# Kernel tuning notes

Measured on AMD Instinct MI355X. Metric: run time of the kernel, lower is better.

Reference implementation:

```python
import jax, jax.numpy as jnp
import numpy as np

DIM = 64
NUM_NODES = 64
SEQ_LEN = 256
BATCH = 64


def setup_inputs() -> dict:
    key = jax.random.key(0)
    ks = jax.random.split(key, 8)
    D = DIM
    x = jax.random.normal(ks[0], (SEQ_LEN, BATCH, NUM_NODES, D), dtype=jnp.float32)
    mask = jnp.ones((SEQ_LEN,), dtype=jnp.int32)
    # msg MLP: Linear(3D -> D) + GELU
    lim_msg = 1.0 / np.sqrt(3 * D)
    msg_W = jax.random.uniform(ks[1], (D, 3 * D), minval=-lim_msg, maxval=lim_msg, dtype=jnp.float32)
    msg_b = jax.random.uniform(ks[2], (D,), minval=-lim_msg, maxval=lim_msg, dtype=jnp.float32)
    # GRUCell(input=D, hidden=D); torch init U(-1/sqrt(hidden), 1/sqrt(hidden))
    lim_g = 1.0 / np.sqrt(D)
    W_ih = jax.random.uniform(ks[3], (3 * D, D), minval=-lim_g, maxval=lim_g, dtype=jnp.float32)
    W_hh = jax.random.uniform(ks[4], (3 * D, D), minval=-lim_g, maxval=lim_g, dtype=jnp.float32)
    b_ih = jax.random.uniform(ks[5], (3 * D,), minval=-lim_g, maxval=lim_g, dtype=jnp.float32)
    b_hh = jax.random.uniform(ks[6], (3 * D,), minval=-lim_g, maxval=lim_g, dtype=jnp.float32)
    # TimeEncode params
    basis_freq = jnp.asarray(1.0 / 10.0 ** np.linspace(0, 9, D), dtype=jnp.float32)
    phase = jnp.zeros((D,), dtype=jnp.float32)
    return {"x": x, "mask": mask, "msg_W": msg_W, "msg_b": msg_b,
            "W_ih": W_ih, "W_hh": W_hh, "b_ih": b_ih, "b_hh": b_hh,
            "basis_freq": basis_freq, "phase": phase}


def _forward(x, mask, msg_W, msg_b, W_ih, W_hh, b_ih, b_hh, basis_freq, phase):
    T, B, C, D = x.shape
    # TimeEncode: cos(t * freq + phase) -> [T, D]
    ts = jnp.arange(T, dtype=jnp.float32)[:, None]
    t_enc = jnp.cos(ts * basis_freq[None, :] + phase[None, :])
    # init_func == 'mean': mean over time -> [B, C, D] -> [B*C, D]
    s0 = jnp.mean(x, axis=0).reshape(B * C, D)
    # time_range = arange(T) * mask (gather indices)
    tr = jnp.arange(T) * mask.astype(jnp.int32)
    x_seq = x[tr].reshape(T, B * C, D)      # gathered timesteps
    te_seq = t_enc[tr]                       # [T, D]

    def step(s, inp):
        xt, tt = inp                        # xt: [B*C, D], tt: [D]
        tt_b = jnp.broadcast_to(tt[None, :], xt.shape)
        cat = jnp.concatenate([xt, s, tt_b], axis=-1)  # [B*C, 3D]
        msg = jax.nn.gelu(cat @ msg_W.T + msg_b, approximate=False)
        # GRUCell (torch gate order: r, z, n)
        gi = msg @ W_ih.T + b_ih
        gh = s @ W_hh.T + b_hh
        i_r, i_z, i_n = jnp.split(gi, 3, axis=-1)
        h_r, h_z, h_n = jnp.split(gh, 3, axis=-1)
        r = jax.nn.sigmoid(i_r + h_r)
        z = jax.nn.sigmoid(i_z + h_z)
        n = jnp.tanh(i_n + r * h_n)
        s_new = (1.0 - z) * n + z * s
        return s_new, s_new

    _, states = jax.lax.scan(step, s0, (x_seq, te_seq))
    return states.reshape(T, B, C, D)


def reference(x, mask, msg_W, msg_b, W_ih, W_hh, b_ih, b_hh, basis_freq, phase):
    return _forward(x, mask, msg_W, msg_b, W_ih, W_hh, b_ih, b_hh, basis_freq, phase)
```

## Files before the change

kernel.cpp:

```cpp
#include <hip/hip_runtime.h>
#include <math.h>

#define DD    64
#define TT    256
#define NROW  4096
#define BLK   512
#define GRID  256

typedef __attribute__((ext_vector_type(8))) short  short8;
typedef __attribute__((ext_vector_type(4))) float  f32x4;

#define BARRIER() do {                                        \
    asm volatile("s_waitcnt lgkmcnt(0)" ::: "memory");        \
    __builtin_amdgcn_sched_barrier(0);                        \
    __builtin_amdgcn_s_barrier();                             \
    __builtin_amdgcn_sched_barrier(0);                        \
  } while (0)

__device__ __forceinline__ unsigned short f2bf(float f) {
  unsigned u = __builtin_bit_cast(unsigned, f);
  u += 0x7fffu + ((u >> 16) & 1u);
  return (unsigned short)(u >> 16);
}

__device__ __forceinline__ unsigned long long pack4(float4 v) {
  return (unsigned long long)f2bf(v.x)
       | ((unsigned long long)f2bf(v.y) << 16)
       | ((unsigned long long)f2bf(v.z) << 32)
       | ((unsigned long long)f2bf(v.w) << 48);
}

__device__ __forceinline__ short8 load_wfrag(const float* p) {
  float4 a = *(const float4*)p;
  float4 b = *(const float4*)(p + 4);
  short8 r;
  r[0] = (short)f2bf(a.x); r[1] = (short)f2bf(a.y);
  r[2] = (short)f2bf(a.z); r[3] = (short)f2bf(a.w);
  r[4] = (short)f2bf(b.x); r[5] = (short)f2bf(b.y);
  r[6] = (short)f2bf(b.z); r[7] = (short)f2bf(b.w);
  return r;
}

__device__ __forceinline__ float fsigmoid(float x) {
  return __builtin_amdgcn_rcpf(1.0f + __expf(-x));
}
__device__ __forceinline__ float ftanh(float x) {
  return 1.0f - 2.0f * __builtin_amdgcn_rcpf(1.0f + __expf(2.0f * x));
}
__device__ __forceinline__ float ferf(float x) {
  float ax = fabsf(x);
  float t  = __builtin_amdgcn_rcpf(fmaf(0.3275911f, ax, 1.0f));
  float p  = fmaf(1.061405429f, t, -1.453152027f);
  p = fmaf(p, t, 1.421413741f);
  p = fmaf(p, t, -0.284496736f);
  p = fmaf(p, t, 0.254829592f);
  p = p * t;
  float y = 1.0f - p * __expf(-ax * ax);
  return copysignf(y, x);
}

__global__ void bias_kernel(const float* __restrict__ msg_W,
                            const float* __restrict__ msg_b,
                            const float* __restrict__ freq,
                            const float* __restrict__ phase,
                            float* __restrict__ bias_t) {
  __shared__ float teL[DD];
  const int t = blockIdx.x;
  const int j = threadIdx.x;
  teL[j] = cosf(fmaf((float)t, freq[j], phase[j]));
  __syncthreads();
  float acc = msg_b[j];
  const float* wrow = msg_W + j * 192 + 128;
  #pragma unroll 8
  for (int k = 0; k < DD; ++k) acc = fmaf(teL[k], wrow[k], acc);
  bias_t[t * DD + j] = acc;
}

__launch_bounds__(BLK, 1)
__global__ void scan5(const float* __restrict__ x,
                      const int*   __restrict__ mask,
                      const float* __restrict__ msg_W,
                      const float* __restrict__ W_ih,
                      const float* __restrict__ W_hh,
                      const float* __restrict__ b_ih,
                      const float* __restrict__ b_hh,
                      const float* __restrict__ bias_t,
                      float* __restrict__ out) {
  __shared__ alignas(16) unsigned short xs[2][16 * 72];
  __shared__ alignas(16) unsigned short ss[16 * 72];
  __shared__ alignas(16) unsigned short ms[16 * 72];
  __shared__ alignas(16) float s0a[16 * 68];
  __shared__ alignas(16) float ghl[16 * 260];
  __shared__ int tr_lds[TT + 2];

  const int tid  = threadIdx.x;
  const int lane = tid & 63;
  const int wv   = tid >> 6;
  const int grp  = wv >> 2;
  const int w4   = wv & 3;
  const int col  = lane & 15;
  const int kh   = lane >> 4;
  const int n    = w4 * 16 + col;
  const int row0 = blockIdx.x * 16;

  if (tid < TT) tr_lds[tid] = tid * mask[tid];
  else if (tid < TT + 2) tr_lds[tid] = 0;

  short8 wm[4], wi[3][2], wh[3][2];
  float bsum01[2] = {0.f, 0.f}, bih2 = 0.f, bhh2 = 0.f;
  if (grp == 0) {
    const float* mrow = msg_W + (size_t)n * 192;
    #pragma unroll
    for (int kf = 0; kf < 4; ++kf) wm[kf] = load_wfrag(mrow + kf * 32 + kh * 8);
    #pragma unroll
    for (int p = 0; p < 3; ++p) {
      const float* irow = W_ih + (size_t)(p * 64 + n) * 64;
      #pragma unroll
      for (int kf = 0; kf < 2; ++kf) wi[p][kf] = load_wfrag(irow + kf * 32 + kh * 8);
    }
    bsum01[0] = b_ih[n]      + b_hh[n];
    bsum01[1] = b_ih[64 + n] + b_hh[64 + n];
    bih2 = b_ih[128 + n];
    bhh2 = b_hh[128 + n];
  } else {
    #pragma unroll
    for (int p = 0; p < 3; ++p) {
      const float* hrow = W_hh + (size_t)(p * 64 + n) * 64;
      #pragma unroll
      for (int kf = 0; kf < 2; ++kf) wh[p][kf] = load_wfrag(hrow + kf * 32 + kh * 8);
    }
  }

  {
    const int half = tid >> 8, rem = tid & 255;
    const int fr = rem >> 4, fd = (rem & 15) * 4;
    const float* px = x + ((size_t)half * 128) * (NROW * DD)
                        + (size_t)(row0 + fr) * DD + fd;
    float4 acc = {0.f, 0.f, 0.f, 0.f};
    #pragma unroll 4
    for (int tl = 0; tl < 128; ++tl) {
      float4 v = *(const float4*)(px + (size_t)tl * (NROW * DD));
      acc.x += v.x; acc.y += v.y; acc.z += v.z; acc.w += v.w;
    }
    float* dst = (half == 0) ? &s0a[fr * 68 + fd] : &ghl[fr * 68 + fd];
    *(float4*)dst = acc;
  }
  __syncthreads();
  if (tid < 256) {
    const int fr = tid >> 4, fd = (tid & 15) * 4;
    float4 a = *(const float4*)&s0a[fr * 68 + fd];
    float4 b = *(const float4*)&ghl[fr * 68 + fd];
    const float inv = 1.0f / 256.0f;
    float4 m = { (a.x + b.x) * inv, (a.y + b.y) * inv,
                 (a.z + b.z) * inv, (a.w + b.w) * inv };
    *(float4*)&s0a[fr * 68 + fd] = m;
    *(unsigned long long*)&ss[fr * 72 + fd] = pack4(m);
    float4 xv0 = *(const float4*)(x + (size_t)(row0 + fr) * DD + fd);
    *(unsigned long long*)&xs[0][fr * 72 + fd] = pack4(xv0);
  }
  __syncthreads();

  float s_reg[4] = {0.f, 0.f, 0.f, 0.f};
  float btc = 0.f;
  if (grp == 0) {
    #pragma unroll
    for (int i = 0; i < 4; ++i) s_reg[i] = s0a[(kh * 4 + i) * 68 + n];
    btc = bias_t[n];
    __builtin_amdgcn_s_setprio(1);
  }

  const int t1  = tid & 255;
  const int fr1 = t1 >> 4;
  const int fd1 = (t1 & 15) * 4;
  float4 xv = {0.f, 0.f, 0.f, 0.f};
  if (grp == 1)
    xv = *(const float4*)(x + ((size_t)tr_lds[1] * NROW + row0 + fr1) * DD + fd1);

  for (int t = 0; t < TT; ++t) {
    if (grp == 0) {
      const unsigned short* ax = &xs[t & 1][(lane & 15) * 72];
      const unsigned short* as = &ss[(lane & 15) * 72];
      short8 xa0 = *(const short8*)(ax + kh * 8);
      short8 xa1 = *(const short8*)(ax + 32 + kh * 8);
      short8 sa0 = *(const short8*)(as + kh * 8);
      short8 sa1 = *(const short8*)(as + 32 + kh * 8);
      float btn = 0.f;
      if (t + 1 < TT) btn = bias_t[tr_lds[t + 1] * DD + n];
      f32x4 amx = {0.f, 0.f, 0.f, 0.f};
      amx = __builtin_amdgcn_mfma_f32_16x16x32_bf16(xa0, wm[0], amx, 0, 0, 0);
      amx = __builtin_amdgcn_mfma_f32_16x16x32_bf16(xa1, wm[1], amx, 0, 0, 0);
      f32x4 ams = {0.f, 0.f, 0.f, 0.f};
      ams = __builtin_amdgcn_mfma_f32_16x16x32_bf16(sa0, wm[2], ams, 0, 0, 0);
      ams = __builtin_amdgcn_mfma_f32_16x16x32_bf16(sa1, wm[3], ams, 0, 0, 0);
      #pragma unroll
      for (int i = 0; i < 4; ++i) {
        float a = amx[i] + ams[i] + btc;
        float g = 0.5f * a * (1.0f + ferf(a * 0.70710678118654752f));
        ms[(kh * 4 + i) * 72 + n] = f2bf(g);
      }
      btc = btn;
    } else {
      if (t + 1 < TT)
        *(unsigned long long*)&xs[(t + 1) & 1][fr1 * 72 + fd1] = pack4(xv);
      if (t + 2 < TT)
        xv = *(const float4*)(x + ((size_t)tr_lds[t + 2] * NROW + row0 + fr1) * DD + fd1);
      const unsigned short* as = &ss[(lane & 15) * 72];
      short8 sa0 = *(const short8*)(as + kh * 8);
      short8 sa1 = *(const short8*)(as + 32 + kh * 8);
      f32x4 agh[3];
      #pragma unroll
      for (int p = 0; p < 3; ++p) {
        f32x4 c = {0.f, 0.f, 0.f, 0.f};
        c = __builtin_amdgcn_mfma_f32_16x16x32_bf16(sa0, wh[p][0], c, 0, 0, 0);
        c = __builtin_amdgcn_mfma_f32_16x16x32_bf16(sa1, wh[p][1], c, 0, 0, 0);
        agh[p] = c;
      }
      #pragma unroll
      for (int i = 0; i < 4; ++i) {
        float4 gv = { agh[0][i], agh[1][i], agh[2][i], 0.f };
        *(float4*)&ghl[(kh * 4 + i) * 260 + n * 4] = gv;
      }
    }
    BARRIER();

    if (grp == 0) {
      const unsigned short* am = &ms[(lane & 15) * 72];
      short8 ma0 = *(const short8*)(am + kh * 8);
      short8 ma1 = *(const short8*)(am + 32 + kh * 8);
      f32x4 agi[3];
      #pragma unroll
      for (int p = 0; p < 3; ++p) {
        f32x4 c = {0.f, 0.f, 0.f, 0.f};
        c = __builtin_amdgcn_mfma_f32_16x16x32_bf16(ma0, wi[p][0], c, 0, 0, 0);
        c = __builtin_amdgcn_mfma_f32_16x16x32_bf16(ma1, wi[p][1], c, 0, 0, 0);
        agi[p] = c;
      }
      #pragma unroll
      for (int i = 0; i < 4; ++i) {
        const int rr = kh * 4 + i;
        float4 gh4 = *(const float4*)&ghl[rr * 260 + n * 4];
        float gr  = agi[0][i] + gh4.x + bsum01[0];
        float gz  = agi[1][i] + gh4.y + bsum01[1];
        float gni = agi[2][i] + bih2;
        float gnh = gh4.z + bhh2;
        float rg = fsigmoid(gr);
        float zg = fsigmoid(gz);
        float ng = ftanh(fmaf(rg, gnh, gni));
        float sn = fmaf(zg, s_reg[i] - ng, ng);
        s_reg[i] = sn;
        ss[rr * 72 + n] = f2bf(sn);
        out[((size_t)t * NROW + row0 + rr) * DD + n] = sn;
      }
    }
    BARRIER();
  }
}

extern "C" void kernel_launch(void* const* d_in, const int* in_sizes, int n_in,
                              void* d_out, int out_size, void* d_ws, size_t ws_size,
                              hipStream_t stream) {
  const float* x      = (const float*)d_in[0];
  const int*   mask   = (const int*)  d_in[1];
  const float* msg_W  = (const float*)d_in[2];
  const float* msg_b  = (const float*)d_in[3];
  const float* W_ih   = (const float*)d_in[4];
  const float* W_hh   = (const float*)d_in[5];
  const float* b_ih   = (const float*)d_in[6];
  const float* b_hh   = (const float*)d_in[7];
  const float* freq   = (const float*)d_in[8];
  const float* phase  = (const float*)d_in[9];
  float* out    = (float*)d_out;
  float* bias_t = (float*)d_ws;

  (void)in_sizes; (void)n_in; (void)out_size; (void)ws_size;

  bias_kernel<<<TT, DD, 0, stream>>>(msg_W, msg_b, freq, phase, bias_t);
  scan5<<<GRID, BLK, 0, stream>>>(x, mask, msg_W, W_ih, W_hh,
                                  b_ih, b_hh, bias_t, out);
}
```

Measured before the change: 345.7 us.

## Halve rows per block to double grid, stage outputs through LDS for coalesced stores

Each block now handles 8 rows instead of 16, doubling the grid to 512 blocks so more CUs get work. MFMA tiles stay 16 rows wide, with the upper 8 rows zero-padded. Output stores move from scattered per-element writes in the GRU wave group to coalesced float4 writes by the second wave group, one step later, read from an fp32 LDS copy of the state. The x prefetch moves after the first barrier and drops double buffering. Half of the MFMA work is wasted on padding, and occupancy now depends on register and LDS limits under launch_bounds(512,4).

```diff
diff --git a/kernel.cpp b/kernel.cpp
--- a/kernel.cpp
+++ b/kernel.cpp
@@ -4,8 +4,9 @@
 #define DD    64
 #define TT    256
 #define NROW  4096
+#define RV    8
 #define BLK   512
-#define GRID  256
+#define GRID  (NROW / RV)
 
 typedef __attribute__((ext_vector_type(8))) short  short8;
 typedef __attribute__((ext_vector_type(4))) float  f32x4;
@@ -76,8 +77,8 @@
   bias_t[t * DD + j] = acc;
 }
 
-__launch_bounds__(BLK, 1)
-__global__ void scan5(const float* __restrict__ x,
+__launch_bounds__(BLK, 4)
+__global__ void scan6(const float* __restrict__ x,
                       const int*   __restrict__ mask,
                       const float* __restrict__ msg_W,
                       const float* __restrict__ W_ih,
@@ -86,7 +87,7 @@
                       const float* __restrict__ b_hh,
                       const float* __restrict__ bias_t,
                       float* __restrict__ out) {
-  __shared__ alignas(16) unsigned short xs[2][16 * 72];
+  __shared__ alignas(16) unsigned short xs[16 * 72];
   __shared__ alignas(16) unsigned short ss[16 * 72];
   __shared__ alignas(16) unsigned short ms[16 * 72];
   __shared__ alignas(16) float s0a[16 * 68];
@@ -101,7 +102,7 @@
   const int col  = lane & 15;
   const int kh   = lane >> 4;
   const int n    = w4 * 16 + col;
-  const int row0 = blockIdx.x * 16;
+  const int row0 = blockIdx.x * RV;
 
   if (tid < TT) tr_lds[tid] = tid * mask[tid];
   else if (tid < TT + 2) tr_lds[tid] = 0;
@@ -132,31 +133,39 @@
   }
 
   {
-    const int half = tid >> 8, rem = tid & 255;
-    const int fr = rem >> 4, fd = (rem & 15) * 4;
-    const float* px = x + ((size_t)half * 128) * (NROW * DD)
+    const int q = tid >> 7, u = tid & 127;
+    const int fr = u >> 4, fd = (u & 15) * 4;
+    const float* px = x + ((size_t)(q * 64)) * (NROW * DD)
                         + (size_t)(row0 + fr) * DD + fd;
     float4 acc = {0.f, 0.f, 0.f, 0.f};
     #pragma unroll 4
-    for (int tl = 0; tl < 128; ++tl) {
+    for (int tl = 0; tl < 64; ++tl) {
       float4 v = *(const float4*)(px + (size_t)tl * (NROW * DD));
       acc.x += v.x; acc.y += v.y; acc.z += v.z; acc.w += v.w;
     }
-    float* dst = (half == 0) ? &s0a[fr * 68 + fd] : &ghl[fr * 68 + fd];
-    *(float4*)dst = acc;
+    *(float4*)&ghl[(q * 128 + u) * 4] = acc;
   }
   __syncthreads();
-  if (tid < 256) {
+  if (tid < 128) {
     const int fr = tid >> 4, fd = (tid & 15) * 4;
-    float4 a = *(const float4*)&s0a[fr * 68 + fd];
-    float4 b = *(const float4*)&ghl[fr * 68 + fd];
+    float4 a = *(const float4*)&ghl[tid * 4];
+    float4 b = *(const float4*)&ghl[(128 + tid) * 4];
+    float4 c = *(const float4*)&ghl[(256 + tid) * 4];
+    float4 d = *(const float4*)&ghl[(384 + tid) * 4];
     const float inv = 1.0f / 256.0f;
-    float4 m = { (a.x + b.x) * inv, (a.y + b.y) * inv,
-                 (a.z + b.z) * inv, (a.w + b.w) * inv };
+    float4 m = { (a.x + b.x + c.x + d.x) * inv, (a.y + b.y + c.y + d.y) * inv,
+                 (a.z + b.z + c.z + d.z) * inv, (a.w + b.w + c.w + d.w) * inv };
     *(float4*)&s0a[fr * 68 + fd] = m;
     *(unsigned long long*)&ss[fr * 72 + fd] = pack4(m);
     float4 xv0 = *(const float4*)(x + (size_t)(row0 + fr) * DD + fd);
-    *(unsigned long long*)&xs[0][fr * 72 + fd] = pack4(xv0);
+    *(unsigned long long*)&xs[fr * 72 + fd] = pack4(xv0);
+  } else if (tid < 256) {
+    const int u2 = tid - 128;
+    const int fr = 8 + (u2 >> 4), fd = (u2 & 15) * 4;
+    float4 z = {0.f, 0.f, 0.f, 0.f};
+    *(float4*)&s0a[fr * 68 + fd] = z;
+    *(unsigned long long*)&ss[fr * 72 + fd] = 0ull;
+    *(unsigned long long*)&xs[fr * 72 + fd] = 0ull;
   }
   __syncthreads();
 
@@ -173,12 +182,12 @@
   const int fr1 = t1 >> 4;
   const int fd1 = (t1 & 15) * 4;
   float4 xv = {0.f, 0.f, 0.f, 0.f};
-  if (grp == 1)
+  if (grp == 1 && t1 < 128)
     xv = *(const float4*)(x + ((size_t)tr_lds[1] * NROW + row0 + fr1) * DD + fd1);
 
   for (int t = 0; t < TT; ++t) {
     if (grp == 0) {
-      const unsigned short* ax = &xs[t & 1][(lane & 15) * 72];
+      const unsigned short* ax = &xs[(lane & 15) * 72];
       const unsigned short* as = &ss[(lane & 15) * 72];
       short8 xa0 = *(const short8*)(ax + kh * 8);
       short8 xa1 = *(const short8*)(ax + 32 + kh * 8);
@@ -200,10 +209,6 @@
       }
       btc = btn;
     } else {
-      if (t + 1 < TT)
-        *(unsigned long long*)&xs[(t + 1) & 1][fr1 * 72 + fd1] = pack4(xv);
-      if (t + 2 < TT)
-        xv = *(const float4*)(x + ((size_t)tr_lds[t + 2] * NROW + row0 + fr1) * DD + fd1);
       const unsigned short* as = &ss[(lane & 15) * 72];
       short8 sa0 = *(const short8*)(as + kh * 8);
       short8 sa1 = *(const short8*)(as + 32 + kh * 8);
@@ -219,6 +224,10 @@
       for (int i = 0; i < 4; ++i) {
         float4 gv = { agh[0][i], agh[1][i], agh[2][i], 0.f };
         *(float4*)&ghl[(kh * 4 + i) * 260 + n * 4] = gv;
+      }
+      if (t > 0 && t1 < 128) {
+        float4 ov = *(const float4*)&s0a[fr1 * 68 + fd1];
+        *(float4*)(out + ((size_t)(t - 1) * NROW + row0 + fr1) * DD + fd1) = ov;
       }
     }
     BARRIER();
@@ -248,11 +257,23 @@
         float ng = ftanh(fmaf(rg, gnh, gni));
         float sn = fmaf(zg, s_reg[i] - ng, ng);
         s_reg[i] = sn;
-        ss[rr * 72 + n] = f2bf(sn);
-        out[((size_t)t * NROW + row0 + rr) * DD + n] = sn;
+        ss[rr * 72 + n]  = f2bf(sn);
+        s0a[rr * 68 + n] = sn;
+      }
+    } else {
+      if (t1 < 128) {
+        if (t + 1 < TT)
+          *(unsigned long long*)&xs[fr1 * 72 + fd1] = pack4(xv);
+        if (t + 2 < TT)
+          xv = *(const float4*)(x + ((size_t)tr_lds[t + 2] * NROW + row0 + fr1) * DD + fd1);
       }
     }
     BARRIER();
+  }
+
+  if (grp == 1 && t1 < 128) {
+    float4 ov = *(const float4*)&s0a[fr1 * 68 + fd1];
+    *(float4*)(out + ((size_t)(TT - 1) * NROW + row0 + fr1) * DD + fd1) = ov;
   }
 }
 
@@ -275,6 +296,6 @@
   (void)in_sizes; (void)n_in; (void)out_size; (void)ws_size;
 
   bias_kernel<<<TT, DD, 0, stream>>>(msg_W, msg_b, freq, phase, bias_t);
-  scan5<<<GRID, BLK, 0, stream>>>(x, mask, msg_W, W_ih, W_hh,
+  scan6<<<GRID, BLK, 0, stream>>>(x, mask, msg_W, W_ih, W_hh,
                                   b_ih, b_hh, bias_t, out);
 }
```

After: 377.6 us. +9.2%, slower.

## Move x-projection MFMA and output stores to the second wave group, off the critical path

Applied to the files above, without the earlier changes.

The input projection x_t·W_x plus time bias is now computed by the W_hh wave group one step ahead, during the second phase, and handed over through shared memory. The message phase then only runs the state-dependent MFMAs. Output stores move from scattered per-element writes in the critical group to coalesced float4 writes by the other group, delayed by one step via an fp32 state copy in shared memory. This shortens the serial dependency chain in each recurrent step, at the cost of extra shared-memory traffic.

```diff
diff --git a/kernel.cpp b/kernel.cpp
--- a/kernel.cpp
+++ b/kernel.cpp
@@ -23,22 +23,26 @@
   return (unsigned short)(u >> 16);
 }
 
-__device__ __forceinline__ unsigned long long pack4(float4 v) {
-  return (unsigned long long)f2bf(v.x)
-       | ((unsigned long long)f2bf(v.y) << 16)
-       | ((unsigned long long)f2bf(v.z) << 32)
-       | ((unsigned long long)f2bf(v.w) << 48);
+__device__ __forceinline__ unsigned long long pack4(f32x4 v) {
+  return (unsigned long long)f2bf(v[0])
+       | ((unsigned long long)f2bf(v[1]) << 16)
+       | ((unsigned long long)f2bf(v[2]) << 32)
+       | ((unsigned long long)f2bf(v[3]) << 48);
+}
+
+__device__ __forceinline__ short8 pack_frag(f32x4 a, f32x4 b) {
+  short8 r;
+  r[0] = (short)f2bf(a[0]); r[1] = (short)f2bf(a[1]);
+  r[2] = (short)f2bf(a[2]); r[3] = (short)f2bf(a[3]);
+  r[4] = (short)f2bf(b[0]); r[5] = (short)f2bf(b[1]);
+  r[6] = (short)f2bf(b[2]); r[7] = (short)f2bf(b[3]);
+  return r;
 }
 
 __device__ __forceinline__ short8 load_wfrag(const float* p) {
-  float4 a = *(const float4*)p;
-  float4 b = *(const float4*)(p + 4);
-  short8 r;
-  r[0] = (short)f2bf(a.x); r[1] = (short)f2bf(a.y);
-  r[2] = (short)f2bf(a.z); r[3] = (short)f2bf(a.w);
-  r[4] = (short)f2bf(b.x); r[5] = (short)f2bf(b.y);
-  r[6] = (short)f2bf(b.z); r[7] = (short)f2bf(b.w);
-  return r;
+  f32x4 a = *(const f32x4*)p;
+  f32x4 b = *(const f32x4*)(p + 4);
+  return pack_frag(a, b);
 }
 
 __device__ __forceinline__ float fsigmoid(float x) {
@@ -77,7 +81,7 @@
 }
 
 __launch_bounds__(BLK, 1)
-__global__ void scan5(const float* __restrict__ x,
+__global__ void scan7(const float* __restrict__ x,
                       const int*   __restrict__ mask,
                       const float* __restrict__ msg_W,
                       const float* __restrict__ W_ih,
@@ -86,12 +90,12 @@
                       const float* __restrict__ b_hh,
                       const float* __restrict__ bias_t,
                       float* __restrict__ out) {
-  __shared__ alignas(16) unsigned short xs[2][16 * 72];
   __shared__ alignas(16) unsigned short ss[16 * 72];
   __shared__ alignas(16) unsigned short ms[16 * 72];
+  __shared__ alignas(16) float amxl[64 * 20];
+  __shared__ alignas(16) float ghl[16 * 260];
   __shared__ alignas(16) float s0a[16 * 68];
-  __shared__ alignas(16) float ghl[16 * 260];
-  __shared__ int tr_lds[TT + 2];
+  __shared__ int tr_lds[TT];
 
   const int tid  = threadIdx.x;
   const int lane = tid & 63;
@@ -104,14 +108,13 @@
   const int row0 = blockIdx.x * 16;
 
   if (tid < TT) tr_lds[tid] = tid * mask[tid];
-  else if (tid < TT + 2) tr_lds[tid] = 0;
-
-  short8 wm[4], wi[3][2], wh[3][2];
+
+  short8 ws[2], wi[3][2], wh[3][2], wx[2];
   float bsum01[2] = {0.f, 0.f}, bih2 = 0.f, bhh2 = 0.f;
   if (grp == 0) {
     const float* mrow = msg_W + (size_t)n * 192;
-    #pragma unroll
-    for (int kf = 0; kf < 4; ++kf) wm[kf] = load_wfrag(mrow + kf * 32 + kh * 8);
+    ws[0] = load_wfrag(mrow + 64 + kh * 8);
+    ws[1] = load_wfrag(mrow + 96 + kh * 8);
     #pragma unroll
     for (int p = 0; p < 3; ++p) {
       const float* irow = W_ih + (size_t)(p * 64 + n) * 64;
@@ -123,6 +126,9 @@
     bih2 = b_ih[128 + n];
     bhh2 = b_hh[128 + n];
   } else {
+    const float* mrow = msg_W + (size_t)n * 192;
+    wx[0] = load_wfrag(mrow + kh * 8);
+    wx[1] = load_wfrag(mrow + 32 + kh * 8);
     #pragma unroll
     for (int p = 0; p < 3; ++p) {
       const float* hrow = W_hh + (size_t)(p * 64 + n) * 64;
@@ -136,74 +142,74 @@
     const int fr = rem >> 4, fd = (rem & 15) * 4;
     const float* px = x + ((size_t)half * 128) * (NROW * DD)
                         + (size_t)(row0 + fr) * DD + fd;
-    float4 acc = {0.f, 0.f, 0.f, 0.f};
+    f32x4 acc = {0.f, 0.f, 0.f, 0.f};
     #pragma unroll 4
     for (int tl = 0; tl < 128; ++tl) {
-      float4 v = *(const float4*)(px + (size_t)tl * (NROW * DD));
-      acc.x += v.x; acc.y += v.y; acc.z += v.z; acc.w += v.w;
-    }
-    float* dst = (half == 0) ? &s0a[fr * 68 + fd] : &ghl[fr * 68 + fd];
-    *(float4*)dst = acc;
+      f32x4 v = *(const f32x4*)(px + (size_t)tl * (NROW * DD));
+      acc += v;
+    }
+    *(f32x4*)&ghl[tid * 4] = acc;
   }
   __syncthreads();
   if (tid < 256) {
     const int fr = tid >> 4, fd = (tid & 15) * 4;
-    float4 a = *(const float4*)&s0a[fr * 68 + fd];
-    float4 b = *(const float4*)&ghl[fr * 68 + fd];
-    const float inv = 1.0f / 256.0f;
-    float4 m = { (a.x + b.x) * inv, (a.y + b.y) * inv,
-                 (a.z + b.z) * inv, (a.w + b.w) * inv };
-    *(float4*)&s0a[fr * 68 + fd] = m;
+    f32x4 a = *(const f32x4*)&ghl[tid * 4];
+    f32x4 b = *(const f32x4*)&ghl[(256 + tid) * 4];
+    f32x4 m = (a + b) * (1.0f / 256.0f);
+    *(f32x4*)&s0a[fr * 68 + fd] = m;
     *(unsigned long long*)&ss[fr * 72 + fd] = pack4(m);
-    float4 xv0 = *(const float4*)(x + (size_t)(row0 + fr) * DD + fd);
-    *(unsigned long long*)&xs[0][fr * 72 + fd] = pack4(xv0);
+  }
+
+  f32x4 xva = {0,0,0,0}, xvb = {0,0,0,0}, xvc = {0,0,0,0}, xvd = {0,0,0,0};
+  if (grp == 1) {
+    const float* px0 = x + (size_t)(row0 + (lane & 15)) * DD + kh * 8;
+    f32x4 f0a = *(const f32x4*)(px0);
+    f32x4 f0b = *(const f32x4*)(px0 + 4);
+    f32x4 f1a = *(const f32x4*)(px0 + 32);
+    f32x4 f1b = *(const f32x4*)(px0 + 36);
+    short8 xa0 = pack_frag(f0a, f0b);
+    short8 xa1 = pack_frag(f1a, f1b);
+    f32x4 c = {0.f, 0.f, 0.f, 0.f};
+    c = __builtin_amdgcn_mfma_f32_16x16x32_bf16(xa0, wx[0], c, 0, 0, 0);
+    c = __builtin_amdgcn_mfma_f32_16x16x32_bf16(xa1, wx[1], c, 0, 0, 0);
+    const float bt = bias_t[n];
+    c[0] += bt; c[1] += bt; c[2] += bt; c[3] += bt;
+    *(f32x4*)&amxl[n * 20 + kh * 4] = c;
+    const float* px1 = x + ((size_t)tr_lds[1] * NROW + row0 + (lane & 15)) * DD + kh * 8;
+    xva = *(const f32x4*)(px1);
+    xvb = *(const f32x4*)(px1 + 4);
+    xvc = *(const f32x4*)(px1 + 32);
+    xvd = *(const f32x4*)(px1 + 36);
   }
   __syncthreads();
 
   float s_reg[4] = {0.f, 0.f, 0.f, 0.f};
-  float btc = 0.f;
   if (grp == 0) {
     #pragma unroll
     for (int i = 0; i < 4; ++i) s_reg[i] = s0a[(kh * 4 + i) * 68 + n];
-    btc = bias_t[n];
     __builtin_amdgcn_s_setprio(1);
   }
 
   const int t1  = tid & 255;
   const int fr1 = t1 >> 4;
   const int fd1 = (t1 & 15) * 4;
-  float4 xv = {0.f, 0.f, 0.f, 0.f};
-  if (grp == 1)
-    xv = *(const float4*)(x + ((size_t)tr_lds[1] * NROW + row0 + fr1) * DD + fd1);
 
   for (int t = 0; t < TT; ++t) {
     if (grp == 0) {
-      const unsigned short* ax = &xs[t & 1][(lane & 15) * 72];
       const unsigned short* as = &ss[(lane & 15) * 72];
-      short8 xa0 = *(const short8*)(ax + kh * 8);
-      short8 xa1 = *(const short8*)(ax + 32 + kh * 8);
       short8 sa0 = *(const short8*)(as + kh * 8);
       short8 sa1 = *(const short8*)(as + 32 + kh * 8);
-      float btn = 0.f;
-      if (t + 1 < TT) btn = bias_t[tr_lds[t + 1] * DD + n];
-      f32x4 amx = {0.f, 0.f, 0.f, 0.f};
-      amx = __builtin_amdgcn_mfma_f32_16x16x32_bf16(xa0, wm[0], amx, 0, 0, 0);
-      amx = __builtin_amdgcn_mfma_f32_16x16x32_bf16(xa1, wm[1], amx, 0, 0, 0);
+      f32x4 am4 = *(const f32x4*)&amxl[n * 20 + kh * 4];
       f32x4 ams = {0.f, 0.f, 0.f, 0.f};
-      ams = __builtin_amdgcn_mfma_f32_16x16x32_bf16(sa0, wm[2], ams, 0, 0, 0);
-      ams = __builtin_amdgcn_mfma_f32_16x16x32_bf16(sa1, wm[3], ams, 0, 0, 0);
+      ams = __builtin_amdgcn_mfma_f32_16x16x32_bf16(sa0, ws[0], ams, 0, 0, 0);
+      ams = __builtin_amdgcn_mfma_f32_16x16x32_bf16(sa1, ws[1], ams, 0, 0, 0);
       #pragma unroll
       for (int i = 0; i < 4; ++i) {
-        float a = amx[i] + ams[i] + btc;
+        float a = ams[i] + am4[i];
         float g = 0.5f * a * (1.0f + ferf(a * 0.70710678118654752f));
         ms[(kh * 4 + i) * 72 + n] = f2bf(g);
       }
-      btc = btn;
     } else {
-      if (t + 1 < TT)
-        *(unsigned long long*)&xs[(t + 1) & 1][fr1 * 72 + fd1] = pack4(xv);
-      if (t + 2 < TT)
-        xv = *(const float4*)(x + ((size_t)tr_lds[t + 2] * NROW + row0 + fr1) * DD + fd1);
       const unsigned short* as = &ss[(lane & 15) * 72];
       short8 sa0 = *(const short8*)(as + kh * 8);
       short8 sa1 = *(const short8*)(as + 32 + kh * 8);
@@ -217,13 +223,21 @@
       }
       #pragma unroll
       for (int i = 0; i < 4; ++i) {
-        float4 gv = { agh[0][i], agh[1][i], agh[2][i], 0.f };
-        *(float4*)&ghl[(kh * 4 + i) * 260 + n * 4] = gv;
+        f32x4 gv = { agh[0][i], agh[1][i], agh[2][i], 0.f };
+        *(f32x4*)&ghl[(kh * 4 + i) * 260 + n * 4] = gv;
+      }
+      if (t > 0) {
+        f32x4 ov = *(const f32x4*)&s0a[fr1 * 68 + fd1];
+        *(f32x4*)(out + ((size_t)(t - 1) * NROW + row0 + fr1) * DD + fd1) = ov;
       }
     }
     BARRIER();
 
     if (grp == 0) {
+      f32x4 gh4[4];
+      #pragma unroll
+      for (int i = 0; i < 4; ++i)
+        gh4[i] = *(const f32x4*)&ghl[(kh * 4 + i) * 260 + n * 4];
       const unsigned short* am = &ms[(lane & 15) * 72];
       short8 ma0 = *(const short8*)(am + kh * 8);
       short8 ma1 = *(const short8*)(am + 32 + kh * 8);
@@ -238,21 +252,43 @@
       #pragma unroll
       for (int i = 0; i < 4; ++i) {
         const int rr = kh * 4 + i;
-        float4 gh4 = *(const float4*)&ghl[rr * 260 + n * 4];
-        float gr  = agi[0][i] + gh4.x + bsum01[0];
-        float gz  = agi[1][i] + gh4.y + bsum01[1];
+        float gr  = agi[0][i] + gh4[i][0] + bsum01[0];
+        float gz  = agi[1][i] + gh4[i][1] + bsum01[1];
         float gni = agi[2][i] + bih2;
-        float gnh = gh4.z + bhh2;
+        float gnh = gh4[i][2] + bhh2;
         float rg = fsigmoid(gr);
         float zg = fsigmoid(gz);
         float ng = ftanh(fmaf(rg, gnh, gni));
         float sn = fmaf(zg, s_reg[i] - ng, ng);
         s_reg[i] = sn;
-        ss[rr * 72 + n] = f2bf(sn);
-        out[((size_t)t * NROW + row0 + rr) * DD + n] = sn;
+        ss[rr * 72 + n]  = f2bf(sn);
+        s0a[rr * 68 + n] = sn;
+      }
+    } else {
+      if (t + 1 < TT) {
+        float bt = bias_t[tr_lds[t + 1] * DD + n];
+        short8 xa0 = pack_frag(xva, xvb);
+        short8 xa1 = pack_frag(xvc, xvd);
+        f32x4 c = {0.f, 0.f, 0.f, 0.f};
+        c = __builtin_amdgcn_mfma_f32_16x16x32_bf16(xa0, wx[0], c, 0, 0, 0);
+        c = __builtin_amdgcn_mfma_f32_16x16x32_bf16(xa1, wx[1], c, 0, 0, 0);
+        c[0] += bt; c[1] += bt; c[2] += bt; c[3] += bt;
+        *(f32x4*)&amxl[n * 20 + kh * 4] = c;
+      }
+      if (t + 2 < TT) {
+        const float* pxn = x + ((size_t)tr_lds[t + 2] * NROW + row0 + (lane & 15)) * DD + kh * 8;
+        xva = *(const f32x4*)(pxn);
+        xvb = *(const f32x4*)(pxn + 4);
+        xvc = *(const f32x4*)(pxn + 32);
+        xvd = *(const f32x4*)(pxn + 36);
       }
     }
     BARRIER();
+  }
+
+  if (grp == 1) {
+    f32x4 ov = *(const f32x4*)&s0a[fr1 * 68 + fd1];
+    *(f32x4*)(out + ((size_t)(TT - 1) * NROW + row0 + fr1) * DD + fd1) = ov;
   }
 }
 
@@ -275,6 +311,6 @@
   (void)in_sizes; (void)n_in; (void)out_size; (void)ws_size;
 
   bias_kernel<<<TT, DD, 0, stream>>>(msg_W, msg_b, freq, phase, bias_t);
-  scan5<<<GRID, BLK, 0, stream>>>(x, mask, msg_W, W_ih, W_hh,
+  scan7<<<GRID, BLK, 0, stream>>>(x, mask, msg_W, W_ih, W_hh,
                                   b_ih, b_hh, bias_t, out);
 }
```

New measurement: 345.3 us. No clear change (-0.1%).
